# Performance work log

Hardware: AMD Instinct MI355X
Metric: run time of the kernel (lower is better)

## Reference

```python
import jax, jax.numpy as jnp
import numpy as np

N_NODES = 100000
N_EDGES = 1600000
F_IN = 128
F_EDGE = 16
HID = 64


def gcn_conv(x, W, b, src, dst, n):
    # PyG GCNConv: add self-loops, symmetric normalization D^-1/2 (A+I) D^-1/2
    h = x @ W  # [N, out]
    loop = jnp.arange(n, dtype=src.dtype)
    src_f = jnp.concatenate([src, loop])
    dst_f = jnp.concatenate([dst, loop])
    ones = jnp.ones(src_f.shape[0], dtype=h.dtype)
    deg = jax.ops.segment_sum(ones, dst_f, num_segments=n)
    dinv = jnp.where(deg > 0, jax.lax.rsqrt(deg), 0.0)
    norm = dinv[src_f] * dinv[dst_f]  # [E+N]
    msg = h[src_f] * norm[:, None]
    out = jax.ops.segment_sum(msg, dst_f, num_segments=n)
    return out + b


def setup_inputs() -> dict:
    key = jax.random.key(0)
    ks = jax.random.split(key, 16)
    g = lambda k, shape, fan_in: jax.random.normal(k, shape, dtype=jnp.float32) * (1.0 / np.sqrt(fan_in))
    inp = {
        "x": jax.random.normal(ks[0], (N_NODES, F_IN), dtype=jnp.float32),
        "edge_index": jax.random.randint(ks[1], (2, N_EDGES), 0, N_NODES, dtype=jnp.int64) if jax.config.read('jax_enable_x64') else jax.random.randint(ks[1], (2, N_EDGES), 0, N_NODES, dtype=jnp.int32),
        "edge_attr": jax.random.normal(ks[2], (N_EDGES, F_EDGE), dtype=jnp.float32),
        # GCN layers
        "W1": g(ks[3], (F_IN, HID), F_IN), "b1": jnp.zeros((HID,), jnp.float32),
        "W2": g(ks[4], (HID, HID), HID), "b2": jnp.zeros((HID,), jnp.float32),
        "W3": g(ks[5], (HID, HID), HID), "b3": jnp.zeros((HID,), jnp.float32),
        # edge MLP: Linear(2*HID+F_EDGE -> HID), Linear(HID -> 32), Linear(32 -> 2)
        "Wm1": g(ks[6], (2 * HID + F_EDGE, HID), 2 * HID + F_EDGE), "bm1": jnp.zeros((HID,), jnp.float32),
        "Wm2": g(ks[7], (HID, 32), HID), "bm2": jnp.zeros((32,), jnp.float32),
        "Wm3": g(ks[8], (32, 2), 32), "bm3": jnp.zeros((2,), jnp.float32),
    }
    return inp


def reference(x, edge_index, edge_attr, W1, b1, W2, b2, W3, b3, Wm1, bm1, Wm2, bm2, Wm3, bm3):
    src, dst = edge_index[0], edge_index[1]
    n = x.shape[0]
    h = jax.nn.relu(gcn_conv(x, W1, b1, src, dst, n))
    h = jax.nn.relu(gcn_conv(h, W2, b2, src, dst, n))
    h = jax.nn.relu(gcn_conv(h, W3, b3, src, dst, n))
    # edge classifier: gather endpoints, concat edge features, small MLP (eval mode -> no dropout)
    e = jnp.concatenate([h[src], h[dst], edge_attr], axis=1)  # [E, 2*HID+F_EDGE]
    e = jax.nn.relu(e @ Wm1 + bm1)
    e = jax.nn.relu(e @ Wm2 + bm2)
    return e @ Wm3 + bm3  # [E, 2]
```

## Files before the change

### kernel.cpp

```cpp
#include <hip/hip_runtime.h>

typedef __attribute__((ext_vector_type(8))) short bf16x8;
typedef __attribute__((ext_vector_type(4))) float f32x4;
typedef __attribute__((ext_vector_type(4))) unsigned int u32x4;

__device__ __forceinline__ short f2bf(float f) {
  unsigned u = __float_as_uint(f);
  u = (u + 0x7fffu + ((u >> 16) & 1u)) >> 16;
  return (short)u;
}
__device__ __forceinline__ float bf2f(unsigned short u) {
  return __uint_as_float(((unsigned)u) << 16);
}
__device__ __forceinline__ unsigned cvtpk(float lo, float hi) {
  unsigned r;
  asm("v_cvt_pk_bf16_f32 %0, %1, %2" : "=v"(r) : "v"(lo), "v"(hi));
  return r;
}
__device__ __forceinline__ bf16x8 u2b(u32x4 w) {
  union { u32x4 u; bf16x8 b; } x; x.u = w; return x.b;
}

__global__ __launch_bounds__(256) void fill_pad_k(const int* __restrict__ src,
                                                  const int* __restrict__ dst,
                                                  unsigned* cursor,
                                                  int* __restrict__ csr_pad, int e, int n) {
  const int part  = blockIdx.x & 7;
  const int lo    = (int)(((long)n * part) >> 3);
  const int hi    = (int)(((long)n * (part + 1)) >> 3);
  const int nb    = gridDim.x >> 3;
  const int brank = blockIdx.x >> 3;
  const long stride = (long)nb * 256;
  for (long i = (long)brank * 256 + threadIdx.x; i < e; i += stride) {
    int d = dst[i];
    if (d >= lo && d < hi) {
      int pos = (int)atomicAdd(&cursor[d], 1u);
      if (pos < 64) csr_pad[((size_t)d << 6) + pos] = src[i];
    }
  }
}

__global__ void dinv_k(const unsigned* __restrict__ deg, float* __restrict__ dinv, int n) {
  int i = blockIdx.x * 256 + threadIdx.x;
  if (i < n) dinv[i] = rsqrtf((float)(deg[i] + 1u));
}

__global__ void pack_all_k(const float* __restrict__ W1, const float* __restrict__ W2,
                           const float* __restrict__ W3, const float* __restrict__ Wm1,
                           const float* __restrict__ Wm2,
                           short* __restrict__ Wn1p, short* __restrict__ Wn2p,
                           short* __restrict__ Wn3p, short* __restrict__ We1p,
                           short* __restrict__ We2p) {
  const int t = blockIdx.x * 256 + threadIdx.x;
  const int stride = gridDim.x * 256;
  auto pack64 = [&](const float* W, short* P, int K, int total) {
    for (int i = t; i < total; i += stride) {
      int j = i & 7, l = (i >> 3) & 63, c = (i >> 9) & 3, kk = i >> 11;
      int row = kk * 32 + ((l >> 4) * 8) + j, col = c * 16 + (l & 15);
      P[i] = f2bf(row < K ? W[row * 64 + col] : 0.f);
    }
  };
  pack64(W1, Wn1p, 128, 8192);
  pack64(W2, Wn2p, 64, 4096);
  pack64(W3, Wn3p, 64, 4096);
  for (int i = t; i < 10240; i += stride) {
    int j = i & 7, l = (i >> 3) & 63, c = (i >> 9) & 3, kk = i >> 11;
    int row = kk * 32 + ((l >> 4) * 8) + j;
    int r_ = l & 15;
    int col = 32 * (c >> 1) + 8 * (r_ >> 2) + 4 * (c & 1) + (r_ & 3);
    We1p[i] = f2bf(row < 144 ? Wm1[row * 64 + col] : 0.f);
  }
  for (int i = t; i < 2048; i += stride) {
    int j = i & 7, l = (i >> 3) & 63, c = (i >> 9) & 1, kk = (i >> 10) & 1;
    int row = kk * 32 + ((l >> 4) * 8) + j, col = c * 16 + (l & 15);
    We2p[i] = f2bf(Wm2[row * 32 + col]);
  }
}

template<int K, bool F32IN>
__global__ __launch_bounds__(256) void node_mfma_k(
    const void* __restrict__ Araw, const short* __restrict__ Wp,
    unsigned short* __restrict__ C, int n)
{
  constexpr int NK = K / 32;
  __shared__ __align__(16) short Wl[NK * 4 * 64 * 8];
  const int tid = threadIdx.x;
  {
    const uint4* s = (const uint4*)Wp; uint4* d = (uint4*)Wl;
    for (int i = tid; i < NK * 4 * 64; i += 256) d[i] = s[i];
  }
  __syncthreads();
  const int lane = tid & 63;
  const int wid  = tid >> 6;
  const int g    = lane >> 4;
  const int r16  = lane & 15;
  const int base = blockIdx.x * 64 + wid * 16;
  if (base >= n) return;
  int arow = base + r16;
  if (arow >= n) arow = n - 1;
  const bf16x8* wb = (const bf16x8*)Wl;
  f32x4 acc[4];
  #pragma unroll
  for (int c = 0; c < 4; ++c) acc[c] = (f32x4){0.f, 0.f, 0.f, 0.f};
  #pragma unroll
  for (int kk = 0; kk < NK; ++kk) {
    bf16x8 a;
    if (F32IN) {
      const float4* af = (const float4*)((const float*)Araw + (size_t)arow * K + kk * 32 + 8 * g);
      float4 u = af[0], v = af[1];
      u32x4 w;
      w[0] = cvtpk(u.x, u.y); w[1] = cvtpk(u.z, u.w);
      w[2] = cvtpk(v.x, v.y); w[3] = cvtpk(v.z, v.w);
      a = u2b(w);
    } else {
      a = ((const bf16x8*)((const unsigned short*)Araw + (size_t)arow * K))[kk * 4 + g];
    }
    #pragma unroll
    for (int c = 0; c < 4; ++c)
      acc[c] = __builtin_amdgcn_mfma_f32_16x16x32_bf16(a, wb[(kk * 4 + c) * 64 + lane], acc[c], 0, 0, 0);
  }
  #pragma unroll
  for (int rr = 0; rr < 4; ++rr) {
    int orow = base + g * 4 + rr;
    if (orow < n) {
      unsigned short* cp = C + (size_t)orow * 64 + r16;
      cp[0]  = (unsigned short)f2bf(acc[0][rr]);
      cp[16] = (unsigned short)f2bf(acc[1][rr]);
      cp[32] = (unsigned short)f2bf(acc[2][rr]);
      cp[48] = (unsigned short)f2bf(acc[3][rr]);
    }
  }
}

__global__ __launch_bounds__(256) void agg_csr_k(
    const unsigned short* __restrict__ lin, const float* __restrict__ dinv,
    const unsigned* __restrict__ deg, const int* __restrict__ csr_pad,
    const float* __restrict__ bias, unsigned short* __restrict__ out, int n)
{
  const int node = blockIdx.x * 4 + (threadIdx.x >> 6);
  if (node >= n) return;
  const int lane = threadIdx.x & 63;
  const int es = lane >> 4;
  const int fq = lane & 15;
  const float dn = dinv[node];
  const int cnt = (int)deg[node];
  const int* sp = csr_pad + ((size_t)node << 6);
  float ax = 0.f, ay = 0.f, az = 0.f, aw = 0.f;
  if (es == 0) {
    ushort4 v = *(const ushort4*)(lin + (size_t)node * 64 + fq * 4);
    float w = dn * dn;
    ax = w * bf2f(v.x); ay = w * bf2f(v.y); az = w * bf2f(v.z); aw = w * bf2f(v.w);
  }
  #pragma unroll 4
  for (int j = es; j < cnt; j += 4) {
    int s = sp[j];
    float w = dinv[s] * dn;
    ushort4 v = *(const ushort4*)(lin + (size_t)s * 64 + fq * 4);
    ax += w * bf2f(v.x); ay += w * bf2f(v.y);
    az += w * bf2f(v.z); aw += w * bf2f(v.w);
  }
  ax += __shfl_xor(ax, 16, 64); ax += __shfl_xor(ax, 32, 64);
  ay += __shfl_xor(ay, 16, 64); ay += __shfl_xor(ay, 32, 64);
  az += __shfl_xor(az, 16, 64); az += __shfl_xor(az, 32, 64);
  aw += __shfl_xor(aw, 16, 64); aw += __shfl_xor(aw, 32, 64);
  if (es == 0) {
    float4 b = *(const float4*)(bias + fq * 4);
    ushort4 o;
    o.x = (unsigned short)f2bf(fmaxf(ax + b.x, 0.f));
    o.y = (unsigned short)f2bf(fmaxf(ay + b.y, 0.f));
    o.z = (unsigned short)f2bf(fmaxf(az + b.z, 0.f));
    o.w = (unsigned short)f2bf(fmaxf(aw + b.w, 0.f));
    *(ushort4*)(out + (size_t)node * 64 + fq * 4) = o;
  }
}

__global__ __launch_bounds__(256, 2) void edge_mlp_mfma_k(
    const unsigned short* __restrict__ hb, const float* __restrict__ ea,
    const int* __restrict__ src, const int* __restrict__ dst,
    const short* __restrict__ W1p, const short* __restrict__ W2p,
    const float* __restrict__ bm1, const float* __restrict__ bm2,
    const float* __restrict__ Wm3, const float* __restrict__ bm3,
    float* __restrict__ out, int E, int ntiles)
{
  const int tid  = threadIdx.x;
  const int lane = tid & 63;
  const int wid  = tid >> 6;
  const int g    = lane >> 4;
  const int r16  = lane & 15;

  bf16x8 w1f[20];
  #pragma unroll
  for (int t = 0; t < 20; ++t) w1f[t] = ((const bf16x8*)W1p)[t * 64 + lane];
  bf16x8 w2f[4];
  #pragma unroll
  for (int t = 0; t < 4; ++t) w2f[t] = ((const bf16x8*)W2p)[t * 64 + lane];

  f32x4 b1v[4];
  #pragma unroll
  for (int c = 0; c < 4; ++c) {
    float4 v = *(const float4*)(bm1 + 32 * (c >> 1) + 8 * g + 4 * (c & 1));
    b1v[c] = (f32x4){v.x, v.y, v.z, v.w};
  }
  f32x4 b2v[2];
  #pragma unroll
  for (int c = 0; c < 2; ++c) {
    float4 v = *(const float4*)(bm2 + c * 16 + 4 * g);
    b2v[c] = (f32x4){v.x, v.y, v.z, v.w};
  }
  float4 w3a[2], w3b[2];
  #pragma unroll
  for (int c = 0; c < 2; ++c) {
    w3a[c] = *(const float4*)(Wm3 + (c * 16 + 4 * g) * 2);
    w3b[c] = *(const float4*)(Wm3 + (c * 16 + 4 * g) * 2 + 4);
  }
  const float b30 = bm3[0], b31 = bm3[1];

  const int ngroups = (ntiles + 3) >> 2;
  if (blockIdx.x >= ngroups) return;

  int mye1, sl1, dl1;
  bf16x8 c_a0, c_a1, c_a2, c_a3;
  float4 c_e0, c_e1;
  {
    int e = (blockIdx.x * 4 + wid) * 16 + r16;
    int mye = (e < E) ? e : (E - 1);
    int sl = src[mye], dl = dst[mye];
    const bf16x8* hs = (const bf16x8*)(hb + (size_t)sl * 64);
    c_a0 = hs[g]; c_a1 = hs[4 + g];
    const bf16x8* hd = (const bf16x8*)(hb + (size_t)dl * 64);
    c_a2 = hd[g]; c_a3 = hd[4 + g];
    if (g < 2) {
      const float4* ep = (const float4*)(ea + (size_t)mye * 16 + 8 * g);
      c_e0 = ep[0]; c_e1 = ep[1];
    }
    int grp1 = blockIdx.x + gridDim.x;
    if (grp1 > ngroups - 1) grp1 = ngroups - 1;
    int e1 = (grp1 * 4 + wid) * 16 + r16;
    mye1 = (e1 < E) ? e1 : (E - 1);
    sl1 = src[mye1]; dl1 = dst[mye1];
  }

  for (int grp = blockIdx.x; grp < ngroups; grp += gridDim.x) {
    const int e0 = (grp * 4 + wid) * 16;

    bf16x8 n_a0, n_a1, n_a2, n_a3;
    float4 n_e0, n_e1;
    {
      const bf16x8* hs = (const bf16x8*)(hb + (size_t)sl1 * 64);
      n_a0 = hs[g]; n_a1 = hs[4 + g];
      const bf16x8* hd = (const bf16x8*)(hb + (size_t)dl1 * 64);
      n_a2 = hd[g]; n_a3 = hd[4 + g];
      if (g < 2) {
        const float4* ep = (const float4*)(ea + (size_t)mye1 * 16 + 8 * g);
        n_e0 = ep[0]; n_e1 = ep[1];
      }
    }
    int mye2, sl2, dl2;
    {
      int grp2 = grp + 2 * gridDim.x;
      if (grp2 > ngroups - 1) grp2 = ngroups - 1;
      int e2 = (grp2 * 4 + wid) * 16 + r16;
      mye2 = (e2 < E) ? e2 : (E - 1);
      sl2 = src[mye2]; dl2 = dst[mye2];
    }

    bf16x8 a4;
    if (g < 2) {
      u32x4 w;
      w[0] = cvtpk(c_e0.x, c_e0.y); w[1] = cvtpk(c_e0.z, c_e0.w);
      w[2] = cvtpk(c_e1.x, c_e1.y); w[3] = cvtpk(c_e1.z, c_e1.w);
      a4 = u2b(w);
    } else {
      a4 = (bf16x8){0, 0, 0, 0, 0, 0, 0, 0};
    }

    f32x4 acc[4];
    #pragma unroll
    for (int c = 0; c < 4; ++c) acc[c] = b1v[c];
    #pragma unroll
    for (int c = 0; c < 4; ++c) {
      acc[c] = __builtin_amdgcn_mfma_f32_16x16x32_bf16(w1f[0 * 4 + c], c_a0, acc[c], 0, 0, 0);
      acc[c] = __builtin_amdgcn_mfma_f32_16x16x32_bf16(w1f[1 * 4 + c], c_a1, acc[c], 0, 0, 0);
      acc[c] = __builtin_amdgcn_mfma_f32_16x16x32_bf16(w1f[2 * 4 + c], c_a2, acc[c], 0, 0, 0);
      acc[c] = __builtin_amdgcn_mfma_f32_16x16x32_bf16(w1f[3 * 4 + c], c_a3, acc[c], 0, 0, 0);
      acc[c] = __builtin_amdgcn_mfma_f32_16x16x32_bf16(w1f[4 * 4 + c], a4,   acc[c], 0, 0, 0);
    }

    u32x4 x0w, x1w;
    x0w[0] = cvtpk(fmaxf(acc[0][0], 0.f), fmaxf(acc[0][1], 0.f));
    x0w[1] = cvtpk(fmaxf(acc[0][2], 0.f), fmaxf(acc[0][3], 0.f));
    x0w[2] = cvtpk(fmaxf(acc[1][0], 0.f), fmaxf(acc[1][1], 0.f));
    x0w[3] = cvtpk(fmaxf(acc[1][2], 0.f), fmaxf(acc[1][3], 0.f));
    x1w[0] = cvtpk(fmaxf(acc[2][0], 0.f), fmaxf(acc[2][1], 0.f));
    x1w[1] = cvtpk(fmaxf(acc[2][2], 0.f), fmaxf(acc[2][3], 0.f));
    x1w[2] = cvtpk(fmaxf(acc[3][0], 0.f), fmaxf(acc[3][1], 0.f));
    x1w[3] = cvtpk(fmaxf(acc[3][2], 0.f), fmaxf(acc[3][3], 0.f));
    bf16x8 xa0 = u2b(x0w), xa1 = u2b(x1w);

    f32x4 acc2[2];
    #pragma unroll
    for (int c = 0; c < 2; ++c) acc2[c] = b2v[c];
    #pragma unroll
    for (int c = 0; c < 2; ++c) {
      acc2[c] = __builtin_amdgcn_mfma_f32_16x16x32_bf16(w2f[0 * 2 + c], xa0, acc2[c], 0, 0, 0);
      acc2[c] = __builtin_amdgcn_mfma_f32_16x16x32_bf16(w2f[1 * 2 + c], xa1, acc2[c], 0, 0, 0);
    }

    float p0 = 0.f, p1 = 0.f;
    #pragma unroll
    for (int c = 0; c < 2; ++c) {
      float v0 = fmaxf(acc2[c][0], 0.f);
      float v1 = fmaxf(acc2[c][1], 0.f);
      float v2 = fmaxf(acc2[c][2], 0.f);
      float v3 = fmaxf(acc2[c][3], 0.f);
      p0 = fmaf(v0, w3a[c].x, p0); p1 = fmaf(v0, w3a[c].y, p1);
      p0 = fmaf(v1, w3a[c].z, p0); p1 = fmaf(v1, w3a[c].w, p1);
      p0 = fmaf(v2, w3b[c].x, p0); p1 = fmaf(v2, w3b[c].y, p1);
      p0 = fmaf(v3, w3b[c].z, p0); p1 = fmaf(v3, w3b[c].w, p1);
    }
    p0 += __shfl_xor(p0, 16, 64); p0 += __shfl_xor(p0, 32, 64);
    p1 += __shfl_xor(p1, 16, 64); p1 += __shfl_xor(p1, 32, 64);
    if (g == 0) {
      int e = e0 + r16;
      if (e < E) {
        float2 o; o.x = p0 + b30; o.y = p1 + b31;
        *(float2*)(out + (size_t)e * 2) = o;
      }
    }

    c_a0 = n_a0; c_a1 = n_a1; c_a2 = n_a2; c_a3 = n_a3;
    c_e0 = n_e0; c_e1 = n_e1;
    mye1 = mye2; sl1 = sl2; dl1 = dl2;
  }
}

extern "C" void kernel_launch(void* const* d_in, const int* in_sizes, int n_in,
                              void* d_out, int out_size, void* d_ws, size_t ws_size,
                              hipStream_t stream) {
  const float* x   = (const float*)d_in[0];
  const int*   ei  = (const int*)d_in[1];
  const float* ea  = (const float*)d_in[2];
  const float* W1  = (const float*)d_in[3];
  const float* b1  = (const float*)d_in[4];
  const float* W2  = (const float*)d_in[5];
  const float* b2  = (const float*)d_in[6];
  const float* W3  = (const float*)d_in[7];
  const float* b3  = (const float*)d_in[8];
  const float* Wm1 = (const float*)d_in[9];
  const float* bm1 = (const float*)d_in[10];
  const float* Wm2 = (const float*)d_in[11];
  const float* bm2 = (const float*)d_in[12];
  const float* Wm3 = (const float*)d_in[13];
  const float* bm3 = (const float*)d_in[14];

  const int N  = in_sizes[0] / 128;
  const int E  = in_sizes[1] / 2;
  const int* srcp = ei;
  const int* dstp = ei + E;

  float* ws = (float*)d_ws;
  size_t off = 0;
  float*    dinv    = ws + off;               off += (size_t)N;
  unsigned* cursor  = (unsigned*)(ws + off);  off += (size_t)N;
  int*      csr_pad = (int*)(ws + off);       off += (size_t)N * 64;
  unsigned short* lin = (unsigned short*)(ws + off); off += (size_t)N * 32;
  unsigned short* hA  = (unsigned short*)(ws + off); off += (size_t)N * 32;
  unsigned short* hB  = (unsigned short*)(ws + off); off += (size_t)N * 32;
  short* Wn1p = (short*)(ws + off); off += 4096;
  short* Wn2p = (short*)(ws + off); off += 2048;
  short* Wn3p = (short*)(ws + off); off += 2048;
  short* We1p = (short*)(ws + off); off += 5120;
  short* We2p = (short*)(ws + off); off += 1024;

  const int gN    = (N + 255) / 256;
  const int gNode = (N + 63) / 64;
  const int gAgg  = (N + 3) / 4;
  const int ntiles = (E + 15) / 16;

  hipMemsetAsync(cursor, 0, (size_t)N * 4, stream);

  fill_pad_k<<<2048, 256, 0, stream>>>(srcp, dstp, cursor, csr_pad, E, N);
  dinv_k<<<gN, 256, 0, stream>>>(cursor, dinv, N);
  pack_all_k<<<40, 256, 0, stream>>>(W1, W2, W3, Wm1, Wm2, Wn1p, Wn2p, Wn3p, We1p, We2p);

  node_mfma_k<128, true><<<gNode, 256, 0, stream>>>(x, Wn1p, lin, N);
  agg_csr_k<<<gAgg, 256, 0, stream>>>(lin, dinv, cursor, csr_pad, b1, hA, N);
  node_mfma_k<64, false><<<gNode, 256, 0, stream>>>(hA, Wn2p, lin, N);
  agg_csr_k<<<gAgg, 256, 0, stream>>>(lin, dinv, cursor, csr_pad, b2, hB, N);
  node_mfma_k<64, false><<<gNode, 256, 0, stream>>>(hB, Wn3p, lin, N);
  agg_csr_k<<<gAgg, 256, 0, stream>>>(lin, dinv, cursor, csr_pad, b3, hA, N);

  edge_mlp_mfma_k<<<2048, 256, 0, stream>>>(hA, ea, srcp, dstp, We1p, We2p,
      bm1, bm2, Wm3, bm3, (float*)d_out, E, ntiles);
}
```

Baseline: 372.1 us.

## Reorder GCN layers 2-3 as aggregate-then-transform and fuse the GEMM into aggregation

GCN layers 2 and 3 now aggregate neighbour features first and then apply the weight matrix, using the identity A(hW) = (Ah)W. Each layer becomes one fused kernel that gathers into shared memory and then runs an MFMA GEMM with bias and ReLU. This drops a separate node GEMM launch per layer and the round trip of the intermediate linear buffer through memory. The CSR fill kernel also loads dst as int4 vectors, and the edge MLP launch bound is raised to 4 blocks per SM. The reordering changes bf16 rounding points (the aggregate is rounded to bf16 before the GEMM), and the higher occupancy target may cause register spills.

```diff
diff --git a/kernel.cpp b/kernel.cpp
--- a/kernel.cpp
+++ b/kernel.cpp
@@ -31,12 +31,19 @@
   const int nb    = gridDim.x >> 3;
   const int brank = blockIdx.x >> 3;
   const long stride = (long)nb * 256;
-  for (long i = (long)brank * 256 + threadIdx.x; i < e; i += stride) {
+  const int e4 = e >> 2;
+  const int4* dst4 = (const int4*)dst;
+  for (long i = (long)brank * 256 + threadIdx.x; i < e4; i += stride) {
+    int4 d = dst4[i];
+    long eb = i * 4;
+    if (d.x >= lo && d.x < hi) { int p = (int)atomicAdd(&cursor[d.x], 1u); if (p < 64) csr_pad[((size_t)d.x << 6) + p] = src[eb]; }
+    if (d.y >= lo && d.y < hi) { int p = (int)atomicAdd(&cursor[d.y], 1u); if (p < 64) csr_pad[((size_t)d.y << 6) + p] = src[eb + 1]; }
+    if (d.z >= lo && d.z < hi) { int p = (int)atomicAdd(&cursor[d.z], 1u); if (p < 64) csr_pad[((size_t)d.z << 6) + p] = src[eb + 2]; }
+    if (d.w >= lo && d.w < hi) { int p = (int)atomicAdd(&cursor[d.w], 1u); if (p < 64) csr_pad[((size_t)d.w << 6) + p] = src[eb + 3]; }
+  }
+  for (long i = (long)e4 * 4 + (long)brank * 256 + threadIdx.x; i < e; i += stride) {
     int d = dst[i];
-    if (d >= lo && d < hi) {
-      int pos = (int)atomicAdd(&cursor[d], 1u);
-      if (pos < 64) csr_pad[((size_t)d << 6) + pos] = src[i];
-    }
+    if (d >= lo && d < hi) { int p = (int)atomicAdd(&cursor[d], 1u); if (p < 64) csr_pad[((size_t)d << 6) + p] = src[i]; }
   }
 }
 
@@ -174,7 +181,87 @@
   }
 }
 
-__global__ __launch_bounds__(256, 2) void edge_mlp_mfma_k(
+__global__ __launch_bounds__(256) void agg_gemm_k(
+    const unsigned short* __restrict__ h_in, const float* __restrict__ dinv,
+    const unsigned* __restrict__ deg, const int* __restrict__ csr_pad,
+    const short* __restrict__ Wp, const float* __restrict__ bias,
+    unsigned short* __restrict__ h_out, int n)
+{
+  __shared__ __align__(16) short Wl[4096];
+  __shared__ __align__(16) short X[4][16][72];
+  const int tid = threadIdx.x;
+  {
+    const uint4* s = (const uint4*)Wp; uint4* d = (uint4*)Wl;
+    for (int i = tid; i < 512; i += 256) d[i] = s[i];
+  }
+  const int lane = tid & 63;
+  const int wid  = tid >> 6;
+  const int es   = lane >> 4;
+  const int fq   = lane & 15;
+  const int base = blockIdx.x * 64 + wid * 16;
+
+  for (int nd = 0; nd < 16; ++nd) {
+    int node = base + nd;
+    if (node >= n) node = n - 1;
+    const float dn = dinv[node];
+    const int cnt = (int)deg[node];
+    const int* sp = csr_pad + ((size_t)node << 6);
+    float ax = 0.f, ay = 0.f, az = 0.f, aw = 0.f;
+    if (es == 0) {
+      ushort4 v = *(const ushort4*)(h_in + (size_t)node * 64 + fq * 4);
+      float w = dn * dn;
+      ax = w * bf2f(v.x); ay = w * bf2f(v.y); az = w * bf2f(v.z); aw = w * bf2f(v.w);
+    }
+    #pragma unroll 4
+    for (int j = es; j < cnt; j += 4) {
+      int s = sp[j];
+      float w = dinv[s] * dn;
+      ushort4 v = *(const ushort4*)(h_in + (size_t)s * 64 + fq * 4);
+      ax += w * bf2f(v.x); ay += w * bf2f(v.y);
+      az += w * bf2f(v.z); aw += w * bf2f(v.w);
+    }
+    ax += __shfl_xor(ax, 16, 64); ax += __shfl_xor(ax, 32, 64);
+    ay += __shfl_xor(ay, 16, 64); ay += __shfl_xor(ay, 32, 64);
+    az += __shfl_xor(az, 16, 64); az += __shfl_xor(az, 32, 64);
+    aw += __shfl_xor(aw, 16, 64); aw += __shfl_xor(aw, 32, 64);
+    if (es == 0) {
+      ushort4 o;
+      o.x = (unsigned short)f2bf(ax); o.y = (unsigned short)f2bf(ay);
+      o.z = (unsigned short)f2bf(az); o.w = (unsigned short)f2bf(aw);
+      *(ushort4*)&X[wid][nd][fq * 4] = o;
+    }
+  }
+  __syncthreads();
+
+  const int g = es, r16 = fq;
+  float bcol[4];
+  #pragma unroll
+  for (int c = 0; c < 4; ++c) bcol[c] = bias[c * 16 + r16];
+  const bf16x8* wb = (const bf16x8*)Wl;
+  f32x4 acc[4];
+  #pragma unroll
+  for (int c = 0; c < 4; ++c) acc[c] = (f32x4){bcol[c], bcol[c], bcol[c], bcol[c]};
+  #pragma unroll
+  for (int kk = 0; kk < 2; ++kk) {
+    bf16x8 a = *(const bf16x8*)&X[wid][r16][kk * 32 + 8 * g];
+    #pragma unroll
+    for (int c = 0; c < 4; ++c)
+      acc[c] = __builtin_amdgcn_mfma_f32_16x16x32_bf16(a, wb[(kk * 4 + c) * 64 + lane], acc[c], 0, 0, 0);
+  }
+  #pragma unroll
+  for (int rr = 0; rr < 4; ++rr) {
+    int orow = base + g * 4 + rr;
+    if (orow < n) {
+      unsigned short* cp = h_out + (size_t)orow * 64 + r16;
+      cp[0]  = (unsigned short)f2bf(fmaxf(acc[0][rr], 0.f));
+      cp[16] = (unsigned short)f2bf(fmaxf(acc[1][rr], 0.f));
+      cp[32] = (unsigned short)f2bf(fmaxf(acc[2][rr], 0.f));
+      cp[48] = (unsigned short)f2bf(fmaxf(acc[3][rr], 0.f));
+    }
+  }
+}
+
+__global__ __launch_bounds__(256, 4) void edge_mlp_mfma_k(
     const unsigned short* __restrict__ hb, const float* __restrict__ ea,
     const int* __restrict__ src, const int* __restrict__ dst,
     const short* __restrict__ W1p, const short* __restrict__ W2p,
@@ -385,10 +472,8 @@
 
   node_mfma_k<128, true><<<gNode, 256, 0, stream>>>(x, Wn1p, lin, N);
   agg_csr_k<<<gAgg, 256, 0, stream>>>(lin, dinv, cursor, csr_pad, b1, hA, N);
-  node_mfma_k<64, false><<<gNode, 256, 0, stream>>>(hA, Wn2p, lin, N);
-  agg_csr_k<<<gAgg, 256, 0, stream>>>(lin, dinv, cursor, csr_pad, b2, hB, N);
-  node_mfma_k<64, false><<<gNode, 256, 0, stream>>>(hB, Wn3p, lin, N);
-  agg_csr_k<<<gAgg, 256, 0, stream>>>(lin, dinv, cursor, csr_pad, b3, hA, N);
+  agg_gemm_k<<<gNode, 256, 0, stream>>>(hA, dinv, cursor, csr_pad, Wn2p, b2, hB, N);
+  agg_gemm_k<<<gNode, 256, 0, stream>>>(hB, dinv, cursor, csr_pad, Wn3p, b3, hA, N);
 
   edge_mlp_mfma_k<<<2048, 256, 0, stream>>>(hA, ea, srcp, dstp, We1p, We2p,
       bm1, bm2, Wm3, bm3, (float*)d_out, E, ntiles);
```

After: 667.8 us. 79.5% more time.
